# Kernel optimization log

Hardware: AMD Instinct MI355X
Metric: run time of the kernel (lower is better)

The kernel has to match this reference:

```python
import jax, jax.numpy as jnp
import numpy as np

B, S, D, H, E = 256, 256, 512, 512, 512


def setup_inputs() -> dict:
    key = jax.random.key(0)
    ks = jax.random.split(key, 12)
    inv = lambda n: 1.0 / np.sqrt(n)
    inp = {
        "prev_h": jax.random.normal(ks[0], (B, H), jnp.float32),
        "prev_c": jax.random.normal(ks[1], (B, H), jnp.float32),
        "batch_H": jax.random.normal(ks[2], (B, S, D), jnp.float32),
        "char_onehots": jax.nn.one_hot(jax.random.randint(ks[3], (B,), 0, E), E, dtype=jnp.float32),
        # parameters (torch nn.Linear convention: y = x @ W.T + b)
        "W_feat": jax.random.uniform(ks[4], (H, D), jnp.float32, -inv(D), inv(D)),
        "W_hid": jax.random.uniform(ks[5], (H, H), jnp.float32, -inv(H), inv(H)),
        "b_hid": jax.random.uniform(ks[6], (H,), jnp.float32, -inv(H), inv(H)),
        "w_score": jax.random.uniform(ks[7], (H,), jnp.float32, -inv(H), inv(H)),
        "W_ih": jax.random.uniform(ks[8], (4 * H, D + E), jnp.float32, -inv(H), inv(H)),
        "W_hh": jax.random.uniform(ks[9], (4 * H, H), jnp.float32, -inv(H), inv(H)),
        "b_ih": jax.random.uniform(ks[10], (4 * H,), jnp.float32, -inv(H), inv(H)),
        "b_hh": jax.random.uniform(ks[11], (4 * H,), jnp.float32, -inv(H), inv(H)),
    }
    return inp


def reference(prev_h, prev_c, batch_H, char_onehots, W_feat, W_hid, b_hid,
              w_score, W_ih, W_hh, b_ih, b_hh):
    # Bahdanau additive attention
    feat_proj = jnp.einsum('bsd,hd->bsh', batch_H, W_feat)            # [B,S,H]
    hidden_proj = prev_h @ W_hid.T + b_hid                            # [B,H]
    energies = jnp.tanh(feat_proj + hidden_proj[:, None, :]) @ w_score  # [B,S]
    alpha = jax.nn.softmax(energies, axis=1)                          # [B,S]
    context = jnp.einsum('bs,bsd->bd', alpha, batch_H)                # [B,D]
    # LSTMCell step (torch gate order: i, f, g, o)
    x = jnp.concatenate([context, char_onehots], axis=1)              # [B,D+E]
    gates = x @ W_ih.T + b_ih + prev_h @ W_hh.T + b_hh                # [B,4H]
    i, f, g, o = jnp.split(gates, 4, axis=1)
    c_new = jax.nn.sigmoid(f) * prev_c + jax.nn.sigmoid(i) * jnp.tanh(g)
    h_new = jax.nn.sigmoid(o) * jnp.tanh(c_new)
    return h_new, c_new, alpha
```

## Files before the change

kernel.cpp:

```cpp
#include <hip/hip_runtime.h>
#include <hip/hip_bf16.h>

typedef unsigned short u16;
typedef unsigned int u32;
typedef __attribute__((ext_vector_type(8))) short bf16x8;
typedef __attribute__((ext_vector_type(4))) float f32x4;
typedef __attribute__((ext_vector_type(4))) u32 u32x4;

typedef __attribute__((address_space(1))) const void gvoid;
typedef __attribute__((address_space(3))) void svoid;

__device__ __forceinline__ void gload16(const void* g, void* l) {
  __builtin_amdgcn_global_load_lds((gvoid*)g, (svoid*)l, 16, 0, 0);
}

__device__ __forceinline__ u16 f2bf(float x){
  union { float f; unsigned u; } v; v.f = x;
  unsigned r = v.u + 0x7fffu + ((v.u >> 16) & 1u);
  return (u16)(r >> 16);
}
__device__ __forceinline__ u32 cvtpk(float lo, float hi){
  u32 r;
  asm("v_cvt_pk_bf16_f32 %0, %1, %2" : "=v"(r) : "v"(lo), "v"(hi));
  return r;
}
__device__ __forceinline__ float fast_tanh(float x){
  x = fminf(fmaxf(x, -12.f), 12.f);
  float e = __expf(2.f * x);
  return (e - 1.f) / (e + 1.f);
}
__device__ __forceinline__ float fast_sig(float x){
  return 1.f / (1.f + __expf(-x));
}

__global__ __launch_bounds__(256) void prep_kernel(
    const float* __restrict__ Wfeat, const float* __restrict__ Whid,
    const float* __restrict__ Wih,   const float* __restrict__ Whh,
    const float* __restrict__ onehot,const float* __restrict__ prevh,
    const float* __restrict__ bih,   const float* __restrict__ bhh,
    u16* __restrict__ wfeat_b, u16* __restrict__ whid_b,
    u16* __restrict__ wcat, u16* __restrict__ xh, float* __restrict__ biascat)
{
  int idx = (blockIdx.x * 256 + threadIdx.x) * 4;
  const float* src;
  u16* dst;
  if (idx < 262144) { src = Wfeat + idx; dst = wfeat_b + idx; }
  else if ((idx -= 262144) < 262144) { src = Whid + idx; dst = whid_b + idx; }
  else if ((idx -= 262144) < 2097152) {
    int r = idx >> 10, k = idx & 1023; src = Wih + idx; dst = wcat + r*1536 + k;
  }
  else if ((idx -= 2097152) < 1048576) {
    int r = idx >> 9, k = idx & 511; src = Whh + idx; dst = wcat + r*1536 + 1024 + k;
  }
  else if ((idx -= 1048576) < 131072) {
    int b = idx >> 9, e = idx & 511; src = onehot + idx; dst = xh + b*1536 + 512 + e;
  }
  else if ((idx -= 131072) < 131072) {
    int b = idx >> 9, h = idx & 511; src = prevh + idx; dst = xh + b*1536 + 1024 + h;
  }
  else {
    idx -= 131072;
    if (idx < 2048) {
      float4 a = *(const float4*)(bih + idx);
      float4 b = *(const float4*)(bhh + idx);
      float4 c = { a.x + b.x, a.y + b.y, a.z + b.z, a.w + b.w };
      *(float4*)(biascat + idx) = c;
    }
    return;
  }
  float4 v = *(const float4*)src;
  ushort4 u;
  u.x = f2bf(v.x); u.y = f2bf(v.y); u.z = f2bf(v.z); u.w = f2bf(v.w);
  *(ushort4*)dst = u;
}

__global__ __launch_bounds__(256) void gemm_btk(
    const u16* __restrict__ Ab, int lda,
    const u16* __restrict__ Wb, int ldw,
    int ksteps, int pstride,
    float* __restrict__ P, int ldc)
{
  __shared__ u16 sA[128][40];
  __shared__ u16 sW[128][40];
  const int tid = threadIdx.x;
  const int lane = tid & 63, wave = tid >> 6;
  const int wr = wave >> 1, wc = wave & 1;
  const int lr = lane & 15, kg = lane >> 4;
  const int m0 = blockIdx.x * 128, n0 = blockIdx.y * 128;
  const int kbase = blockIdx.z * ksteps * 32;
  P += (size_t)blockIdx.z * pstride;
  const int sr = tid >> 1, sh = tid & 1;

  const f32x4 zero = {0.f, 0.f, 0.f, 0.f};
  f32x4 acc[4][4];
  #pragma unroll
  for (int i = 0; i < 4; ++i)
    #pragma unroll
    for (int j = 0; j < 4; ++j)
      acc[i][j] = zero;

  for (int ks = 0; ks < ksteps; ++ks) {
    const int kt = kbase + ks * 32;
    __syncthreads();
    {
      const u16* ap = Ab + (size_t)(m0 + sr) * lda + kt + sh * 16;
      *(bf16x8*)&sA[sr][sh*16]     = *(const bf16x8*)ap;
      *(bf16x8*)&sA[sr][sh*16 + 8] = *(const bf16x8*)(ap + 8);
      const u16* wp = Wb + (size_t)(n0 + sr) * ldw + kt + sh * 16;
      *(bf16x8*)&sW[sr][sh*16]     = *(const bf16x8*)wp;
      *(bf16x8*)&sW[sr][sh*16 + 8] = *(const bf16x8*)(wp + 8);
    }
    __syncthreads();
    bf16x8 af[4], wf[4];
    #pragma unroll
    for (int mi = 0; mi < 4; ++mi) af[mi] = *(const bf16x8*)&sA[wr*64 + mi*16 + lr][kg*8];
    #pragma unroll
    for (int ni = 0; ni < 4; ++ni) wf[ni] = *(const bf16x8*)&sW[wc*64 + ni*16 + lr][kg*8];
    #pragma unroll
    for (int mi = 0; mi < 4; ++mi)
      #pragma unroll
      for (int ni = 0; ni < 4; ++ni)
        acc[mi][ni] = __builtin_amdgcn_mfma_f32_16x16x32_bf16(af[mi], wf[ni], acc[mi][ni], 0, 0, 0);
  }

  #pragma unroll
  for (int ni = 0; ni < 4; ++ni) {
    const int col = n0 + wc*64 + ni*16 + lr;
    #pragma unroll
    for (int mi = 0; mi < 4; ++mi) {
      const int row = m0 + wr*64 + mi*16 + kg*4;
      #pragma unroll
      for (int rr = 0; rr < 4; ++rr)
        P[(size_t)(row + rr) * ldc + col] = acc[mi][ni][rr];
    }
  }
}

__global__ __launch_bounds__(512, 4) void energies_gemm(
    const float* __restrict__ A, const u16* __restrict__ Wb,
    const float* __restrict__ hpp, const float* __restrict__ bhid,
    const float* __restrict__ wsc, float* __restrict__ epart)
{
  __shared__ u16 sA[2][128 * 32];
  __shared__ u16 sW[2][256 * 32];
  const int tid = threadIdx.x;
  const int lane = tid & 63, wv = tid >> 6;
  const int wr = wv >> 2, wc = wv & 3;
  const int lr = lane & 15, kg = lane >> 4;
  const int m0 = blockIdx.x * 128, n0 = blockIdx.y * 256;
  const int b = m0 >> 8;

  const int arow = tid >> 2, achk = tid & 3;
  const float* gA = A + (size_t)(m0 + arow) * 512 + achk * 8;
  const int adst = arow * 32 + ((achk ^ ((arow >> 1) & 3)) * 8);

  const u16* gW0 = Wb + (size_t)(n0 + wv * 16 + (lane >> 2)) * 512 + (lane & 3) * 8;
  const u16* gW1 = gW0 + 128 * 512;
  const int wdst0 = wv * 512;
  const int wdst1 = wdst0 + 4096;

  const f32x4 zero = {0.f, 0.f, 0.f, 0.f};
  f32x4 acc[4][4];
  #pragma unroll
  for (int i = 0; i < 4; ++i)
    #pragma unroll
    for (int j = 0; j < 4; ++j)
      acc[i][j] = zero;

  float4 pa0, pa1, pb0, pb1;

  gload16(gW0, &sW[0][wdst0]);
  gload16(gW1, &sW[0][wdst1]);
  __builtin_amdgcn_sched_barrier(0);
  pa0 = *(const float4*)(gA);       pa1 = *(const float4*)(gA + 4);
  pb0 = *(const float4*)(gA + 32);  pb1 = *(const float4*)(gA + 36);
  __builtin_amdgcn_sched_barrier(0);
  {
    u32x4 c;
    c[0] = cvtpk(pa0.x, pa0.y); c[1] = cvtpk(pa0.z, pa0.w);
    c[2] = cvtpk(pa1.x, pa1.y); c[3] = cvtpk(pa1.z, pa1.w);
    *(u32x4*)&sA[0][adst] = c;
  }
  asm volatile("s_waitcnt lgkmcnt(0)" ::: "memory");
  __builtin_amdgcn_s_barrier();
  __builtin_amdgcn_sched_barrier(0);

  #pragma unroll
  for (int t = 0; t < 16; ++t) {
    const int cur = t & 1, nxt = cur ^ 1;
    if (t < 15) {
      const int kt = (t + 1) * 32;
      gload16(gW0 + kt, &sW[nxt][wdst0]);
      gload16(gW1 + kt, &sW[nxt][wdst1]);
    }
    __builtin_amdgcn_sched_barrier(0);
    if (t < 14) {
      const int kt = (t + 2) * 32;
      if (t & 1) { pb0 = *(const float4*)(gA + kt); pb1 = *(const float4*)(gA + kt + 4); }
      else       { pa0 = *(const float4*)(gA + kt); pa1 = *(const float4*)(gA + kt + 4); }
    }
    __builtin_amdgcn_sched_barrier(0);
    bf16x8 af[4], wf[4];
    #pragma unroll
    for (int mi = 0; mi < 4; ++mi) {
      const int row = wr*64 + mi*16 + lr;
      af[mi] = *(const bf16x8*)&sA[cur][row * 32 + ((kg ^ ((row >> 1) & 3)) * 8)];
    }
    #pragma unroll
    for (int ni = 0; ni < 4; ++ni)
      wf[ni] = *(const bf16x8*)&sW[cur][(wc*64 + ni*16 + lr) * 32 + kg*8];
    #pragma unroll
    for (int mi = 0; mi < 4; ++mi)
      #pragma unroll
      for (int ni = 0; ni < 4; ++ni)
        acc[mi][ni] = __builtin_amdgcn_mfma_f32_16x16x32_bf16(af[mi], wf[ni], acc[mi][ni], 0, 0, 0);
    if (t < 15) {
      u32x4 c;
      if (t & 1) {
        c[0] = cvtpk(pa0.x, pa0.y); c[1] = cvtpk(pa0.z, pa0.w);
        c[2] = cvtpk(pa1.x, pa1.y); c[3] = cvtpk(pa1.z, pa1.w);
      } else {
        c[0] = cvtpk(pb0.x, pb0.y); c[1] = cvtpk(pb0.z, pb0.w);
        c[2] = cvtpk(pb1.x, pb1.y); c[3] = cvtpk(pb1.z, pb1.w);
      }
      *(u32x4*)&sA[nxt][adst] = c;
    }
    if (t < 15) {
      if (t < 14) asm volatile("s_waitcnt vmcnt(2)" ::: "memory");
      else        asm volatile("s_waitcnt vmcnt(0)" ::: "memory");
      asm volatile("s_waitcnt lgkmcnt(0)" ::: "memory");
      __builtin_amdgcn_s_barrier();
      __builtin_amdgcn_sched_barrier(0);
    }
  }

  float hpv[4], wsv[4];
  #pragma unroll
  for (int ni = 0; ni < 4; ++ni) {
    const int col = n0 + wc*64 + ni*16 + lr;
    float h = bhid[col];
    #pragma unroll
    for (int z = 0; z < 4; ++z) h += hpp[z * 131072 + b * 512 + col];
    hpv[ni] = h;
    wsv[ni] = wsc[col];
  }
  const int p = blockIdx.y * 4 + wc;
  #pragma unroll
  for (int mi = 0; mi < 4; ++mi) {
    #pragma unroll
    for (int rr = 0; rr < 4; ++rr) {
      float s = 0.f;
      #pragma unroll
      for (int ni = 0; ni < 4; ++ni)
        s += fast_tanh(acc[mi][ni][rr] + hpv[ni]) * wsv[ni];
      s += __shfl_xor(s, 1, 64);
      s += __shfl_xor(s, 2, 64);
      s += __shfl_xor(s, 4, 64);
      s += __shfl_xor(s, 8, 64);
      if (lr == 0)
        epart[p * 65536 + m0 + wr*64 + mi*16 + kg*4 + rr] = s;
    }
  }
}

__global__ __launch_bounds__(256) void softctx_k(
    const float* __restrict__ epart, const float* __restrict__ H,
    float* __restrict__ alpha, u16* __restrict__ xh)
{
  const int bb = blockIdx.x, t = threadIdx.x;
  float e = 0.f;
  #pragma unroll
  for (int p = 0; p < 8; ++p) e += epart[p * 65536 + bb * 256 + t];
  float mx = e;
  #pragma unroll
  for (int o = 32; o >= 1; o >>= 1) mx = fmaxf(mx, __shfl_xor(mx, o, 64));
  __shared__ float sm[4], ss[4];
  if ((t & 63) == 0) sm[t >> 6] = mx;
  __syncthreads();
  mx = fmaxf(fmaxf(sm[0], sm[1]), fmaxf(sm[2], sm[3]));
  float ex = __expf(e - mx);
  float sum = ex;
  #pragma unroll
  for (int o = 32; o >= 1; o >>= 1) sum += __shfl_xor(sum, o, 64);
  if ((t & 63) == 0) ss[t >> 6] = sum;
  __syncthreads();
  sum = ss[0] + ss[1] + ss[2] + ss[3];
  const float av = ex / sum;
  alpha[bb * 256 + t] = av;
  __shared__ float sal[256];
  sal[t] = av;
  __syncthreads();
  const int q = t >> 6, c = t & 63;
  float a[8];
  #pragma unroll
  for (int j = 0; j < 8; ++j) a[j] = 0.f;
  const float* p = H + (size_t)bb * 131072 + c * 8;
  for (int s = q * 64; s < q * 64 + 64; ++s) {
    float4 v0 = *(const float4*)(p + (size_t)s * 512);
    float4 v1 = *(const float4*)(p + (size_t)s * 512 + 4);
    const float al = sal[s];
    a[0] = fmaf(al, v0.x, a[0]); a[1] = fmaf(al, v0.y, a[1]);
    a[2] = fmaf(al, v0.z, a[2]); a[3] = fmaf(al, v0.w, a[3]);
    a[4] = fmaf(al, v1.x, a[4]); a[5] = fmaf(al, v1.y, a[5]);
    a[6] = fmaf(al, v1.z, a[6]); a[7] = fmaf(al, v1.w, a[7]);
  }
  __shared__ float red[256][8];
  #pragma unroll
  for (int j = 0; j < 8; ++j) red[t][j] = a[j];
  __syncthreads();
  if (q == 0) {
    #pragma unroll
    for (int j = 0; j < 8; ++j) {
      float s = red[t][j] + red[t + 64][j] + red[t + 128][j] + red[t + 192][j];
      xh[bb * 1536 + c * 8 + j] = f2bf(s);
    }
  }
}

__global__ __launch_bounds__(256) void lstm_reduce(
    const float* __restrict__ P, const float* __restrict__ biascat,
    const float* __restrict__ prev_c, float* __restrict__ out)
{
  const int idx = blockIdx.x * 256 + threadIdx.x;
  const int b = idx >> 9, h = idx & 511;
  float gi = biascat[h], gf = biascat[512 + h], gg = biascat[1024 + h], go = biascat[1536 + h];
  #pragma unroll
  for (int z = 0; z < 4; ++z) {
    const float* q = P + (size_t)z * 524288 + (size_t)b * 2048;
    gi += q[h]; gf += q[512 + h]; gg += q[1024 + h]; go += q[1536 + h];
  }
  const float c = fast_sig(gf) * prev_c[idx] + fast_sig(gi) * fast_tanh(gg);
  out[idx] = fast_sig(go) * fast_tanh(c);
  out[131072 + idx] = c;
}

extern "C" void kernel_launch(void* const* d_in, const int* in_sizes, int n_in,
                              void* d_out, int out_size, void* d_ws, size_t ws_size,
                              hipStream_t stream) {
  const float* prev_h  = (const float*)d_in[0];
  const float* prev_c  = (const float*)d_in[1];
  const float* batch_H = (const float*)d_in[2];
  const float* onehot  = (const float*)d_in[3];
  const float* W_feat  = (const float*)d_in[4];
  const float* W_hid   = (const float*)d_in[5];
  const float* b_hid   = (const float*)d_in[6];
  const float* w_score = (const float*)d_in[7];
  const float* W_ih    = (const float*)d_in[8];
  const float* W_hh    = (const float*)d_in[9];
  const float* b_ih    = (const float*)d_in[10];
  const float* b_hh    = (const float*)d_in[11];
  float* out = (float*)d_out;

  char* ws = (char*)d_ws;
  u16*   wfeat_b = (u16*)(ws);
  u16*   whid_b  = (u16*)(ws + 524288);
  u16*   wcat    = (u16*)(ws + 1048576);
  u16*   xh      = (u16*)(ws + 7340032);
  float* biascat = (float*)(ws + 8126464);
  float* hpp     = (float*)(ws + 8134656);
  float* epart   = (float*)(ws + 10231808);
  float* gpart   = (float*)(ws + 12328960);

  float* alpha = out + 262144;

  prep_kernel<<<3842, 256, 0, stream>>>(W_feat, W_hid, W_ih, W_hh, onehot, prev_h,
                                        b_ih, b_hh, wfeat_b, whid_b, wcat, xh, biascat);
  gemm_btk<<<dim3(2, 4, 4), 256, 0, stream>>>(xh + 1024, 1536, whid_b, 512, 4, 131072, hpp, 512);
  energies_gemm<<<dim3(512, 2), 512, 0, stream>>>(batch_H, wfeat_b, hpp, b_hid, w_score, epart);
  softctx_k<<<256, 256, 0, stream>>>(epart, batch_H, alpha, xh);
  gemm_btk<<<dim3(2, 16, 4), 256, 0, stream>>>(xh, 1536, wcat, 1536, 12, 524288, gpart, 2048);
  lstm_reduce<<<512, 256, 0, stream>>>(gpart, biascat, prev_c, out);
}
```

Measured before the change: 118.6 us.

## Split energies GEMM K-step into two prioritized MFMA halves with interleaved loads

Restructures the main K loop of energies_gemm so the 16 MFMAs per step run as two groups of 8, each wrapped in s_setprio and barriers. The next A-tile conversion and prefetch sit between the two groups, and the second pair of W fragments is read from LDS there too. The fixed end-of-iteration wait is replaced by explicit vmcnt waits at the top of the step and before the A conversion. The intent is to overlap global and LDS traffic with matrix work and to keep waves in lockstep. It also lowers the launch-bounds occupancy hint from 4 to 3 to give the compiler more registers, at the cost of fewer resident waves and extra barriers per step.

```diff
diff --git a/kernel.cpp b/kernel.cpp
--- a/kernel.cpp
+++ b/kernel.cpp
@@ -136,7 +136,7 @@
   }
 }
 
-__global__ __launch_bounds__(512, 4) void energies_gemm(
+__global__ __launch_bounds__(512, 3) void energies_gemm(
     const float* __restrict__ A, const u16* __restrict__ Wb,
     const float* __restrict__ hpp, const float* __restrict__ bhid,
     const float* __restrict__ wsc, float* __restrict__ epart)
@@ -155,9 +155,9 @@
   const int adst = arow * 32 + ((achk ^ ((arow >> 1) & 3)) * 8);
 
   const u16* gW0 = Wb + (size_t)(n0 + wv * 16 + (lane >> 2)) * 512 + (lane & 3) * 8;
-  const u16* gW1 = gW0 + 128 * 512;
+  const u16* gW1 = gW0 + (size_t)128 * 512;
   const int wdst0 = wv * 512;
-  const int wdst1 = wdst0 + 4096;
+  const int wdst1 = 4096 + wv * 512;
 
   const f32x4 zero = {0.f, 0.f, 0.f, 0.f};
   f32x4 acc[4][4];
@@ -169,52 +169,55 @@
 
   float4 pa0, pa1, pb0, pb1;
 
+  pa0 = *(const float4*)(gA);
+  pa1 = *(const float4*)(gA + 4);
   gload16(gW0, &sW[0][wdst0]);
   gload16(gW1, &sW[0][wdst1]);
-  __builtin_amdgcn_sched_barrier(0);
-  pa0 = *(const float4*)(gA);       pa1 = *(const float4*)(gA + 4);
-  pb0 = *(const float4*)(gA + 32);  pb1 = *(const float4*)(gA + 36);
-  __builtin_amdgcn_sched_barrier(0);
   {
     u32x4 c;
     c[0] = cvtpk(pa0.x, pa0.y); c[1] = cvtpk(pa0.z, pa0.w);
     c[2] = cvtpk(pa1.x, pa1.y); c[3] = cvtpk(pa1.z, pa1.w);
     *(u32x4*)&sA[0][adst] = c;
   }
+  pb0 = *(const float4*)(gA + 32);
+  pb1 = *(const float4*)(gA + 36);
   asm volatile("s_waitcnt lgkmcnt(0)" ::: "memory");
   __builtin_amdgcn_s_barrier();
-  __builtin_amdgcn_sched_barrier(0);
 
   #pragma unroll
   for (int t = 0; t < 16; ++t) {
     const int cur = t & 1, nxt = cur ^ 1;
+    const int kt1 = (t + 1) * 32;
+
     if (t < 15) {
-      const int kt = (t + 1) * 32;
-      gload16(gW0 + kt, &sW[nxt][wdst0]);
-      gload16(gW1 + kt, &sW[nxt][wdst1]);
-    }
-    __builtin_amdgcn_sched_barrier(0);
-    if (t < 14) {
-      const int kt = (t + 2) * 32;
-      if (t & 1) { pb0 = *(const float4*)(gA + kt); pb1 = *(const float4*)(gA + kt + 4); }
-      else       { pa0 = *(const float4*)(gA + kt); pa1 = *(const float4*)(gA + kt + 4); }
-    }
-    __builtin_amdgcn_sched_barrier(0);
-    bf16x8 af[4], wf[4];
+      gload16(gW0 + kt1, &sW[nxt][wdst0]);
+      gload16(gW1 + kt1, &sW[nxt][wdst1]);
+      asm volatile("s_waitcnt vmcnt(4)" ::: "memory");
+    } else {
+      asm volatile("s_waitcnt vmcnt(0)" ::: "memory");
+    }
+    bf16x8 af[4], wf0, wf1, wf2, wf3;
     #pragma unroll
     for (int mi = 0; mi < 4; ++mi) {
       const int row = wr*64 + mi*16 + lr;
       af[mi] = *(const bf16x8*)&sA[cur][row * 32 + ((kg ^ ((row >> 1) & 3)) * 8)];
     }
-    #pragma unroll
-    for (int ni = 0; ni < 4; ++ni)
-      wf[ni] = *(const bf16x8*)&sW[cur][(wc*64 + ni*16 + lr) * 32 + kg*8];
-    #pragma unroll
-    for (int mi = 0; mi < 4; ++mi)
-      #pragma unroll
-      for (int ni = 0; ni < 4; ++ni)
-        acc[mi][ni] = __builtin_amdgcn_mfma_f32_16x16x32_bf16(af[mi], wf[ni], acc[mi][ni], 0, 0, 0);
+    wf0 = *(const bf16x8*)&sW[cur][(wc*64 +  0 + lr) * 32 + kg*8];
+    wf1 = *(const bf16x8*)&sW[cur][(wc*64 + 16 + lr) * 32 + kg*8];
+    __builtin_amdgcn_s_barrier();
+    asm volatile("s_waitcnt lgkmcnt(0)" ::: "memory");
+    __builtin_amdgcn_sched_barrier(0);
+    __builtin_amdgcn_s_setprio(1);
+    #pragma unroll
+    for (int mi = 0; mi < 4; ++mi) {
+      acc[mi][0] = __builtin_amdgcn_mfma_f32_16x16x32_bf16(af[mi], wf0, acc[mi][0], 0, 0, 0);
+      acc[mi][1] = __builtin_amdgcn_mfma_f32_16x16x32_bf16(af[mi], wf1, acc[mi][1], 0, 0, 0);
+    }
+    __builtin_amdgcn_s_setprio(0);
+    __builtin_amdgcn_s_barrier();
+
     if (t < 15) {
+      asm volatile("s_waitcnt vmcnt(2)" ::: "memory");
       u32x4 c;
       if (t & 1) {
         c[0] = cvtpk(pa0.x, pa0.y); c[1] = cvtpk(pa0.z, pa0.w);
@@ -224,14 +227,25 @@
         c[2] = cvtpk(pb1.x, pb1.y); c[3] = cvtpk(pb1.z, pb1.w);
       }
       *(u32x4*)&sA[nxt][adst] = c;
-    }
-    if (t < 15) {
-      if (t < 14) asm volatile("s_waitcnt vmcnt(2)" ::: "memory");
-      else        asm volatile("s_waitcnt vmcnt(0)" ::: "memory");
-      asm volatile("s_waitcnt lgkmcnt(0)" ::: "memory");
-      __builtin_amdgcn_s_barrier();
-      __builtin_amdgcn_sched_barrier(0);
-    }
+      if (t < 14) {
+        const int kt2 = (t + 2) * 32;
+        if (t & 1) { pb0 = *(const float4*)(gA + kt2); pb1 = *(const float4*)(gA + kt2 + 4); }
+        else       { pa0 = *(const float4*)(gA + kt2); pa1 = *(const float4*)(gA + kt2 + 4); }
+      }
+    }
+    wf2 = *(const bf16x8*)&sW[cur][(wc*64 + 32 + lr) * 32 + kg*8];
+    wf3 = *(const bf16x8*)&sW[cur][(wc*64 + 48 + lr) * 32 + kg*8];
+    __builtin_amdgcn_s_barrier();
+    asm volatile("s_waitcnt lgkmcnt(0)" ::: "memory");
+    __builtin_amdgcn_sched_barrier(0);
+    __builtin_amdgcn_s_setprio(1);
+    #pragma unroll
+    for (int mi = 0; mi < 4; ++mi) {
+      acc[mi][2] = __builtin_amdgcn_mfma_f32_16x16x32_bf16(af[mi], wf2, acc[mi][2], 0, 0, 0);
+      acc[mi][3] = __builtin_amdgcn_mfma_f32_16x16x32_bf16(af[mi], wf3, acc[mi][3], 0, 0, 0);
+    }
+    __builtin_amdgcn_s_setprio(0);
+    if (t < 15) __builtin_amdgcn_s_barrier();
   }
 
   float hpv[4], wsv[4];
```

Result: no change. 119.1 us (+0.5%).
